# Kernel tuning notes

Measured on AMD Instinct MI355X. Metric: run time of the kernel, lower is better.

## Reference

```python
import jax, jax.numpy as jnp
import numpy as np

K = 3          # kernel size
SH, SW = 2, 1  # stride
PH, PW = 1, 1  # padding


def conv2d(x, w, b, stride, pad):
    y = jax.lax.conv_general_dilated(
        x, w, window_strides=stride,
        padding=[(pad[0], pad[0]), (pad[1], pad[1])],
        dimension_numbers=('NCHW', 'OIHW', 'NCHW'))
    return y + b[None, :, None, None]


def setup_inputs() -> dict:
    key = jax.random.key(0)
    ks = jax.random.split(key, 4)
    x = jax.random.normal(ks[0], (8, 64, 128, 128), jnp.float32)
    # scale offset weights small so sampled offsets are O(1) pixels (exercises
    # the bilinear path without sampling far out of bounds)
    w_offset = jax.random.normal(ks[1], (18, 64, 3, 3), jnp.float32) * 0.02
    b_offset = jnp.zeros((18,), jnp.float32)
    w_mask = jax.random.normal(ks[2], (9, 64, 3, 3), jnp.float32) * 0.05
    b_mask = jnp.zeros((9,), jnp.float32)
    w_conv = jax.random.normal(ks[3], (64, 64, 3, 3), jnp.float32) * (1.0 / 24.0)
    return dict(x=x, w_offset=w_offset, b_offset=b_offset,
                w_mask=w_mask, b_mask=b_mask, w_conv=w_conv)


def _bilinear_gather(x, py, px):
    # x: [B,C,H,W]; py, px: [B,K2,Ho,Wo] float sampling coordinates.
    # Zero-padding outside the image (torchvision deform_conv2d semantics).
    B, C, H, W = x.shape
    y0f = jnp.floor(py)
    x0f = jnp.floor(px)
    dy = py - y0f
    dx = px - x0f
    y0 = y0f.astype(jnp.int32)
    x0 = x0f.astype(jnp.int32)

    def corner(yi, xi, wgt):
        valid = (yi >= 0) & (yi < H) & (xi >= 0) & (xi < W)
        yc = jnp.clip(yi, 0, H - 1)
        xc = jnp.clip(xi, 0, W - 1)
        # per-batch fancy gather -> [B, C, K2, Ho, Wo]
        g = jax.vmap(lambda xb, yb, xbi: xb[:, yb, xbi])(x, yc, xc)
        return g * (wgt * valid)[:, None]

    return (corner(y0,     x0,     (1 - dy) * (1 - dx))
            + corner(y0,     x0 + 1, (1 - dy) * dx)
            + corner(y0 + 1, x0,     dy * (1 - dx))
            + corner(y0 + 1, x0 + 1, dy * dx))


def reference(x, w_offset, b_offset, w_mask, b_mask, w_conv):
    B, C, H, W = x.shape
    offset = conv2d(x, w_offset, b_offset, (SH, SW), (PH, PW))   # [B, 2*K2, Ho, Wo]
    mask = jax.nn.sigmoid(conv2d(x, w_mask, b_mask, (SH, SW), (PH, PW)))  # [B, K2, Ho, Wo]
    Ho, Wo = offset.shape[2], offset.shape[3]
    K2 = K * K
    off = offset.reshape(B, K2, 2, Ho, Wo)
    off_y = off[:, :, 0]   # [B,K2,Ho,Wo]
    off_x = off[:, :, 1]
    ky = (jnp.arange(K2) // K).astype(jnp.float32)
    kx = (jnp.arange(K2) % K).astype(jnp.float32)
    hs = (jnp.arange(Ho) * SH - PH).astype(jnp.float32)
    ws = (jnp.arange(Wo) * SW - PW).astype(jnp.float32)
    py = off_y + ky[None, :, None, None] + hs[None, None, :, None]
    px = off_x + kx[None, :, None, None] + ws[None, None, None, :]
    sampled = _bilinear_gather(x, py, px) * mask[:, None]  # [B,C,K2,Ho,Wo]
    # weighted accumulate over in-channels and kernel taps
    out = jnp.einsum('ock,bckhw->bohw', w_conv.reshape(-1, C, K2), sampled)
    return out
```

## Files before the change

### kernel.cpp

```cpp
#include <hip/hip_runtime.h>
#include <hip/hip_fp16.h>
#include <math.h>

#define BB 8
#define CC 64
#define HH 128
#define WW 128
#define HO 64
#define WO 128
#define OC 64
#define HW (HH * WW)

typedef __attribute__((ext_vector_type(4))) float floatx4;
typedef __attribute__((ext_vector_type(8))) _Float16 half8;

__device__ __forceinline__ unsigned short f2h(float f) {
    __half h = __float2half(f);
    return __builtin_bit_cast(unsigned short, h);
}
__device__ __forceinline__ unsigned int packpair(float a, float b) {
    __half2 h = __floats2half2_rn(a, b);
    return __builtin_bit_cast(unsigned int, h);
}
__device__ __forceinline__ void lgkm_barrier() {
    asm volatile("s_waitcnt lgkmcnt(0)" ::: "memory");
    __builtin_amdgcn_s_barrier();
}

__global__ __launch_bounds__(256) void prep(
    const float* __restrict__ x,
    const float* __restrict__ w_off, const float* __restrict__ w_msk,
    const float* __restrict__ w_conv,
    unsigned int* __restrict__ xP,
    unsigned short* __restrict__ Wom, unsigned short* __restrict__ W2)
{
    __shared__ float T[64][77];
    int tid = threadIdx.x, bx = blockIdx.x;
    if (bx < 2048) {
        int wh = bx & 1, b = (bx >> 1) & 7, y = bx >> 4;
        int w0 = wh << 6;
        const float* xb = x + (((size_t)b * CC) * HH + y) * WW + w0;
#pragma unroll
        for (int i = 0; i < 4; ++i) {
            int idx = i * 256 + tid;
            int cch = idx >> 4, f4 = (idx & 15) << 2;
            floatx4 v = *(const floatx4*)(xb + (size_t)cch * HW + f4);
            T[cch][f4 + 0] = v.x;
            T[cch][f4 + 1] = v.y;
            T[cch][f4 + 2] = v.z;
            T[cch][f4 + 3] = v.w;
        }
        if (tid < 64) {
            float e = 0.0f;
            if (w0 + 64 < WW) e = xb[(size_t)tid * HW + 64];
            T[tid][64] = e;
        }
        __syncthreads();
        int ch = tid & 63;
        int wb = (tid >> 6) << 4;
        size_t base = ((((size_t)b * HH + y) * WW) + w0 + wb) * 64 + ch;
#pragma unroll
        for (int j = 0; j < 4; ++j) {
            int wl = wb + 4 * j;
            float a0 = T[ch][wl + 0];
            float a1 = T[ch][wl + 1];
            float a2 = T[ch][wl + 2];
            float a3 = T[ch][wl + 3];
            float a4 = T[ch][wl + 4];
            xP[base + (size_t)(4 * j + 0) * 64] = packpair(a0, a1);
            xP[base + (size_t)(4 * j + 1) * 64] = packpair(a1, a2);
            xP[base + (size_t)(4 * j + 2) * 64] = packpair(a2, a3);
            xP[base + (size_t)(4 * j + 3) * 64] = packpair(a3, a4);
        }
    } else if (bx < 2120) {
        int i = (bx - 2048) * 256 + tid;
        int chn = i / 576, kk = i % 576;
        int xs = kk >> 6, cc = kk & 63;
        float v = 0.0f;
        if (chn < 18)      v = w_off[(chn * CC + cc) * 9 + xs];
        else if (chn < 27) v = w_msk[((chn - 18) * CC + cc) * 9 + xs];
        Wom[i] = f2h(v);
    } else {
        int i = (bx - 2120) * 256 + tid;
        int k = i % 9, cc = (i / 9) % CC, o = i / (CC * 9);
        W2[((size_t)k * OC + o) * CC + cc] = f2h(w_conv[i]);
    }
}

__global__ __launch_bounds__(256, 4) void fused(
    const unsigned int* __restrict__ xP,
    const unsigned short* __restrict__ Wom, const unsigned short* __restrict__ W2,
    const float* __restrict__ b_off, const float* __restrict__ b_msk,
    float* __restrict__ out)
{
    __shared__ __align__(16) char lds[18304];
    typedef _Float16 XsRow[34][72];
    XsRow* Xs = (XsRow*)lds;
    unsigned short (*S)[32][64] = (unsigned short(*)[32][64])lds;
    uint2* metaC = (uint2*)(lds + 8192);
    uint2* metaR = (uint2*)(lds + 10496);
    float (*omr)[33] = (float(*)[33])(lds + 14720);

    int tid = threadIdx.x;
    int lane = tid & 63;
    int wv = __builtin_amdgcn_readfirstlane(tid >> 6);
    int bx = blockIdx.x;
    int b = bx & 7;
    int rest = bx >> 3;
    int h = rest >> 2;
    int w0 = (rest & 3) * 32;
    int h2 = 2 * h - 1;
    int m16 = lane & 15, q = lane >> 4;

    const unsigned int* xPb_u = xP + (size_t)b * HW * 64;

    for (int u = tid; u < 1632; u += 256) {
        int ky = u / 544;
        int rem = u - ky * 544;
        int col = rem >> 4, c4 = rem & 15;
        int hy = h2 + ky, wc = w0 - 1 + col;
        unsigned int lo0 = 0u, lo1 = 0u;
        if ((unsigned)hy < (unsigned)HH && (unsigned)wc < (unsigned)WW) {
            const uint4 g = *(const uint4*)(xPb_u + ((size_t)hy * WW + wc) * 64 + c4 * 4);
            lo0 = (g.x & 0xffffu) | (g.y << 16);
            lo1 = (g.z & 0xffffu) | (g.w << 16);
        }
        uint2* dst = (uint2*)((unsigned short*)lds + ((ky * 34 + col) * 72 + c4 * 4));
        *dst = make_uint2(lo0, lo1);
    }
    lgkm_barrier();

    {
        int mt = wv & 1, nt = wv >> 1;
        floatx4 a = (floatx4){0.f, 0.f, 0.f, 0.f};
        const _Float16* wa = (const _Float16*)Wom + (mt * 16 + m16) * 576 + q * 8;
#pragma unroll
        for (int t = 0; t < 18; ++t) {
            int xs = t >> 1, ky = xs / 3, kx = xs % 3;
            half8 af = *(const half8*)(wa + t * 32);
            half8 bf = *(const half8*)&Xs[ky][nt * 16 + m16 + kx][(t & 1) * 32 + q * 8];
            a = __builtin_amdgcn_mfma_f32_16x16x32_f16(af, bf, a, 0, 0, 0);
        }
#pragma unroll
        for (int r = 0; r < 4; ++r) {
            int chn = mt * 16 + q * 4 + r;
            if (chn < 27) omr[chn][nt * 16 + m16] = a[r];
        }
    }
    lgkm_barrier();

    for (int u = tid; u < 288; u += 256) {
        int kk = u >> 5, pos = u & 31;
        float offy = omr[2 * kk][pos] + b_off[2 * kk];
        float offx = omr[2 * kk + 1][pos] + b_off[2 * kk + 1];
        float mk = 1.0f / (1.0f + __expf(-(omr[18 + kk][pos] + b_msk[kk])));
        float py = offy + (float)(kk / 3) + (float)h2;
        float px = offx + (float)(kk % 3) + (float)(w0 + pos - 1);

        float y0f = floorf(py), x0f = floorf(px);
        float dy = py - y0f, dx = px - x0f;
        int y0 = (int)y0f, x0 = (int)x0f;
        int y1 = y0 + 1, x1 = x0 + 1;
        bool vy0 = (unsigned)y0 < (unsigned)HH;
        bool vy1 = (unsigned)y1 < (unsigned)HH;
        bool vx0 = (unsigned)x0 < (unsigned)WW;
        bool vx1 = (unsigned)x1 < (unsigned)WW;
        float w00 = (1.0f - dy) * (1.0f - dx) * ((vy0 && vx0) ? mk : 0.0f);
        float w01 = (1.0f - dy) * dx          * ((vy0 && vx1) ? mk : 0.0f);
        float w10 = dy * (1.0f - dx)          * ((vy1 && vx0) ? mk : 0.0f);
        float w11 = dy * dx                   * ((vy1 && vx1) ? mk : 0.0f);
        int xbase = min(max(x0, 0), WW - 2);
        bool s0 = x0 > xbase;
        bool s1 = x1 > xbase;
        float cxA = (s0 ? 0.f : w00) + (s1 ? 0.f : w01);
        float cyA = (s0 ? w00 : 0.f) + (s1 ? w01 : 0.f);
        float cxB = (s0 ? 0.f : w10) + (s1 ? 0.f : w11);
        float cyB = (s0 ? w10 : 0.f) + (s1 ? w11 : 0.f);
        int yc0 = min(max(y0, 0), HH - 1);
        int yc1 = min(max(y1, 0), HH - 1);

        __half2 hA = __floats2half2_rn(cxA, cyA);
        __half2 hB = __floats2half2_rn(cxB, cyB);
        metaC[u] = make_uint2(__builtin_bit_cast(unsigned int, hA),
                              __builtin_bit_cast(unsigned int, hB));
        metaR[u] = make_uint2((unsigned)(yc0 * WW + xbase) * 256u,
                              (unsigned)(yc1 * WW + xbase) * 256u);
    }
    lgkm_barrier();

    int p0 = wv * 8;
    const char* xPb = (const char*)xPb_u;
    unsigned int voff = 4u * (unsigned)lane;
    floatx4 acc0 = (floatx4){0.f, 0.f, 0.f, 0.f};
    floatx4 acc1 = (floatx4){0.f, 0.f, 0.f, 0.f};

    unsigned int Ga0[8], Ga1[8], Gb0[8], Gb1[8];
    half8 afr[3][2];
    const _Float16* W2w = (const _Float16*)W2 + ((size_t)wv * 16 + m16) * CC + q * 8;

    auto loadaf = [&](int k, int slot) {
#pragma unroll
        for (int s = 0; s < 2; ++s)
            afr[slot][s] = *(const half8*)(W2w + (size_t)k * (OC * CC) + s * 32);
    };
    auto issue = [&](int k, unsigned int (&A0)[8], unsigned int (&A1)[8]) {
#pragma unroll
        for (int i = 0; i < 8; ++i) {
            uint2 zw = metaR[k * 32 + p0 + i];
            const char* r0 = xPb + (unsigned)__builtin_amdgcn_readfirstlane((int)zw.x);
            const char* r1 = xPb + (unsigned)__builtin_amdgcn_readfirstlane((int)zw.y);
            A0[i] = *(const unsigned int*)(r0 + voff);
            A1[i] = *(const unsigned int*)(r1 + voff);
        }
    };
    auto dostore = [&](int k, int buf, unsigned int (&A0)[8], unsigned int (&A1)[8]) {
#pragma unroll
        for (int i = 0; i < 8; ++i) {
            uint2 cf = metaC[k * 32 + p0 + i];
            __half2 hA = __builtin_bit_cast(__half2, cf.x);
            __half2 hB = __builtin_bit_cast(__half2, cf.y);
            __half2 g0 = __builtin_bit_cast(__half2, A0[i]);
            __half2 g1 = __builtin_bit_cast(__half2, A1[i]);
            __half2 p = __hfma2(hA, g0, __hmul2(hB, g1));
            __half sv = __hadd(__low2half(p), __high2half(p));
            int pos = p0 + i;
            S[buf][pos][((lane >> 3) ^ (pos & 7)) * 8 + (lane & 7)] =
                __builtin_bit_cast(unsigned short, sv);
        }
    };
    auto mfma_step = [&](int k, int buf, int slot) {
#pragma unroll
        for (int s = 0; s < 2; ++s) {
            half8 af = afr[slot][s];
            int cb = ((q + 4 * s) ^ (m16 & 7)) * 8;
            half8 bf0 = *(const half8*)&S[buf][m16][cb];
            half8 bf1 = *(const half8*)&S[buf][16 + m16][cb];
            acc0 = __builtin_amdgcn_mfma_f32_16x16x32_f16(af, bf0, acc0, 0, 0, 0);
            acc1 = __builtin_amdgcn_mfma_f32_16x16x32_f16(af, bf1, acc1, 0, 0, 0);
        }
    };

    loadaf(0, 0);
    loadaf(1, 1);
    issue(0, Ga0, Ga1);
    dostore(0, 0, Ga0, Ga1);
    issue(1, Gb0, Gb1);
#pragma unroll
    for (int k = 0; k < 9; ++k) {
        lgkm_barrier();
        if (k < 7) {
            loadaf(k + 2, (k + 2) % 3);
            if ((k & 1) == 0) issue(k + 2, Ga0, Ga1);
            else              issue(k + 2, Gb0, Gb1);
        }
        mfma_step(k, k & 1, k % 3);
        if (k < 8) {
            if ((k & 1) == 0) dostore(k + 1, 1, Gb0, Gb1);
            else              dostore(k + 1, 0, Ga0, Ga1);
        }
    }

#pragma unroll
    for (int nt = 0; nt < 2; ++nt) {
        floatx4 av = nt ? acc1 : acc0;
#pragma unroll
        for (int r = 0; r < 4; ++r) {
            int o = wv * 16 + q * 4 + r;
            out[(((size_t)b * OC + o) * HO + h) * WO + w0 + nt * 16 + m16] = av[r];
        }
    }
}

extern "C" void kernel_launch(void* const* d_in, const int* in_sizes, int n_in,
                              void* d_out, int out_size, void* d_ws, size_t ws_size,
                              hipStream_t stream)
{
    const float* x      = (const float*)d_in[0];
    const float* w_off  = (const float*)d_in[1];
    const float* b_off  = (const float*)d_in[2];
    const float* w_msk  = (const float*)d_in[3];
    const float* b_msk  = (const float*)d_in[4];
    const float* w_conv = (const float*)d_in[5];
    float* out = (float*)d_out;

    unsigned int* xP = (unsigned int*)d_ws;
    unsigned short* Wom = (unsigned short*)(xP + (size_t)BB * HW * 64);
    unsigned short* W2 = Wom + 32 * 576;

    prep<<<dim3(2264), dim3(256), 0, stream>>>(x, w_off, w_msk, w_conv,
                                               xP, Wom, W2);
    fused<<<dim3(2048), dim3(256), 0, stream>>>(xP, Wom, W2,
                                                b_off, b_msk, out);
}
```

Measured before the change: 141.6 us.

## Transpose prep staging for vectorized xP stores and prefetch gather row offsets

The prep kernel now stores x transposed in shared memory as [w][c], so each thread reads float4 channel groups and writes a 16-byte uint4 of packed half pairs. Previously it wrote 4-byte scattered stores, so this should improve global write coalescing. The fused kernel splits the metaR LDS read and readfirstlane from the global gather issue, fetching row offsets one tap ahead into scalar arrays. This hides LDS latency before the gathers, at the cost of extra register pressure.

```diff
diff --git a/kernel.cpp b/kernel.cpp
--- a/kernel.cpp
+++ b/kernel.cpp
@@ -34,7 +34,7 @@
     unsigned int* __restrict__ xP,
     unsigned short* __restrict__ Wom, unsigned short* __restrict__ W2)
 {
-    __shared__ float T[64][77];
+    __shared__ float T[66][65];
     int tid = threadIdx.x, bx = blockIdx.x;
     if (bx < 2048) {
         int wh = bx & 1, b = (bx >> 1) & 7, y = bx >> 4;
@@ -45,32 +45,31 @@
             int idx = i * 256 + tid;
             int cch = idx >> 4, f4 = (idx & 15) << 2;
             floatx4 v = *(const floatx4*)(xb + (size_t)cch * HW + f4);
-            T[cch][f4 + 0] = v.x;
-            T[cch][f4 + 1] = v.y;
-            T[cch][f4 + 2] = v.z;
-            T[cch][f4 + 3] = v.w;
+            T[f4 + 0][cch] = v.x;
+            T[f4 + 1][cch] = v.y;
+            T[f4 + 2][cch] = v.z;
+            T[f4 + 3][cch] = v.w;
         }
         if (tid < 64) {
             float e = 0.0f;
             if (w0 + 64 < WW) e = xb[(size_t)tid * HW + 64];
-            T[tid][64] = e;
+            T[64][tid] = e;
         }
         __syncthreads();
-        int ch = tid & 63;
-        int wb = (tid >> 6) << 4;
-        size_t base = ((((size_t)b * HH + y) * WW) + w0 + wb) * 64 + ch;
+        int c4 = tid & 15;
+        int wr = tid >> 4;
+        size_t rowbase = (((size_t)b * HH + y) * WW) + w0;
 #pragma unroll
         for (int j = 0; j < 4; ++j) {
-            int wl = wb + 4 * j;
-            float a0 = T[ch][wl + 0];
-            float a1 = T[ch][wl + 1];
-            float a2 = T[ch][wl + 2];
-            float a3 = T[ch][wl + 3];
-            float a4 = T[ch][wl + 4];
-            xP[base + (size_t)(4 * j + 0) * 64] = packpair(a0, a1);
-            xP[base + (size_t)(4 * j + 1) * 64] = packpair(a1, a2);
-            xP[base + (size_t)(4 * j + 2) * 64] = packpair(a2, a3);
-            xP[base + (size_t)(4 * j + 3) * 64] = packpair(a3, a4);
+            int w = 16 * j + wr;
+            floatx4 a  = *(const floatx4*)&T[w][4 * c4];
+            floatx4 bb = *(const floatx4*)&T[w + 1][4 * c4];
+            uint4 d;
+            d.x = packpair(a.x, bb.x);
+            d.y = packpair(a.y, bb.y);
+            d.z = packpair(a.z, bb.z);
+            d.w = packpair(a.w, bb.w);
+            *(uint4*)(xP + (rowbase + w) * 64 + 4 * c4) = d;
         }
     } else if (bx < 2120) {
         int i = (bx - 2048) * 256 + tid;
@@ -198,19 +197,27 @@
     half8 afr[3][2];
     const _Float16* W2w = (const _Float16*)W2 + ((size_t)wv * 16 + m16) * CC + q * 8;
 
+    unsigned sRx[2][8], sRy[2][8];
+
     auto loadaf = [&](int k, int slot) {
 #pragma unroll
         for (int s = 0; s < 2; ++s)
             afr[slot][s] = *(const half8*)(W2w + (size_t)k * (OC * CC) + s * 32);
     };
-    auto issue = [&](int k, unsigned int (&A0)[8], unsigned int (&A1)[8]) {
+    auto fetchMeta = [&](int k, int s) {
 #pragma unroll
         for (int i = 0; i < 8; ++i) {
             uint2 zw = metaR[k * 32 + p0 + i];
-            const char* r0 = xPb + (unsigned)__builtin_amdgcn_readfirstlane((int)zw.x);
-            const char* r1 = xPb + (unsigned)__builtin_amdgcn_readfirstlane((int)zw.y);
-            A0[i] = *(const unsigned int*)(r0 + voff);
-            A1[i] = *(const unsigned int*)(r1 + voff);
+            sRx[s][i] = (unsigned)__builtin_amdgcn_readfirstlane((int)zw.x);
+            sRy[s][i] = (unsigned)__builtin_amdgcn_readfirstlane((int)zw.y);
+        }
+    };
+    auto issue = [&](int k, unsigned int (&A0)[8], unsigned int (&A1)[8]) {
+        int s = k & 1;
+#pragma unroll
+        for (int i = 0; i < 8; ++i) {
+            A0[i] = *(const unsigned int*)(xPb + sRx[s][i] + voff);
+            A1[i] = *(const unsigned int*)(xPb + sRy[s][i] + voff);
         }
     };
     auto dostore = [&](int k, int buf, unsigned int (&A0)[8], unsigned int (&A1)[8]) {
@@ -242,8 +249,11 @@
 
     loadaf(0, 0);
     loadaf(1, 1);
+    fetchMeta(0, 0);
+    fetchMeta(1, 1);
     issue(0, Ga0, Ga1);
     dostore(0, 0, Ga0, Ga1);
+    fetchMeta(2, 0);
     issue(1, Gb0, Gb1);
 #pragma unroll
     for (int k = 0; k < 9; ++k) {
@@ -253,6 +263,7 @@
             if ((k & 1) == 0) issue(k + 2, Ga0, Ga1);
             else              issue(k + 2, Gb0, Gb1);
         }
+        if (k < 6) fetchMeta(k + 3, (k + 3) & 1);
         mfma_step(k, k & 1, k % 3);
         if (k < 8) {
             if ((k & 1) == 0) dostore(k + 1, 1, Gb0, Gb1);
```

New measurement: 142.0 us. No clear change (+0.2%).
